# Performance work log

Hardware: AMD Instinct MI355X
Metric: run time of the kernel (lower is better)

## Reference

```python
import jax, jax.numpy as jnp
import numpy as np

N_HEADS = 8

def setup_inputs() -> dict:
    key = jax.random.key(0)
    qkv = jax.random.normal(key, (4, 1, 3 * N_HEADS * 64, 2048), dtype=jnp.float32)
    return {"qkv": qkv}

def reference(qkv):
    # qkv: [N, G, 3*H*C, T]
    bs, groups, width, length = qkv.shape
    ch = width // (3 * N_HEADS)
    q, k, v = jnp.split(qkv, 3, axis=2)
    scale = 1.0 / np.sqrt(ch)  # applied to BOTH q and k (as in original)
    qr = (q * scale).reshape(bs, groups, N_HEADS, ch, length)
    kr = (k * scale).reshape(bs, groups, N_HEADS, ch, length)
    vr = v.reshape(bs, groups, N_HEADS, ch, length)
    weight = jnp.einsum('bghct,bghcs->bghts', qr, kr)  # [N,G,H,T,T]
    weight = jax.nn.softmax(weight.astype(jnp.float32), axis=-1).astype(qkv.dtype)
    a = jnp.einsum('bghts,bghcs->bghct', weight, vr)  # [N,G,H,C,T]
    return a.reshape(bs, -1, length)  # [N, G*H*C, T]
```

## Files before the change

kernel.cpp:

```cpp
#include <hip/hip_runtime.h>
#include <hip/hip_bf16.h>

typedef __attribute__((ext_vector_type(4))) float f32x4;
typedef __attribute__((ext_vector_type(16))) float f32x16;
typedef __attribute__((ext_vector_type(4))) float f4;
typedef __attribute__((ext_vector_type(8))) short bf16x8;
typedef __attribute__((ext_vector_type(4))) short s16x4;
typedef __attribute__((ext_vector_type(4))) unsigned u32x4;

#define T_LEN 2048
#define SPAD 72
#define QSCALE 0.022542110013890054f

#define SWZ(r) (((r) ^ ((r) >> 3)) & 7)

__device__ inline short f2bf(float f) {
  unsigned u = __builtin_bit_cast(unsigned, f);
  return (short)((u + 0x7fffu + ((u >> 16) & 1u)) >> 16);
}

__global__ __launch_bounds__(256) void prep_t(const float* __restrict__ qkv,
                                              short* __restrict__ qt,
                                              short* __restrict__ kt) {
  __shared__ float tile[64][65];
  const int bid = blockIdx.x;
  const int tch = bid & 31;
  const int head = (bid >> 5) & 31;
  const int sel = bid >> 10;
  const int b = head >> 3, h = head & 7;
  const float* src = qkv + ((size_t)b * 1536 + sel * 512 + h * 64) * T_LEN + tch * 64;
  short* dst = (sel ? kt : qt) + (size_t)head * T_LEN * 64 + (size_t)tch * 64 * 64;
  const int tid = threadIdx.x;
  const float sc = sel ? 1.0f : QSCALE;

  for (int e = tid; e < 4096; e += 256) {
    int c = e >> 6, t = e & 63;
    tile[c][t] = src[(size_t)c * T_LEN + t];
  }
  __syncthreads();
  for (int e = tid; e < 2048; e += 256) {
    int t = e >> 5, c2 = (e & 31) * 2;
    unsigned lo = (unsigned short)f2bf(tile[c2][t] * sc);
    unsigned hi = (unsigned short)f2bf(tile[c2 + 1][t] * sc);
    int cdst = sel ? (c2 ^ (SWZ(t) << 3)) : c2;
    *(unsigned*)&dst[t * 64 + cdst] = lo | (hi << 16);
  }
}

__global__ __launch_bounds__(256) void prep_v(const float* __restrict__ qkv,
                                              short* __restrict__ v_out) {
  int id = blockIdx.x * 256 + threadIdx.x;
  int s4 = id & 15;
  int c = (id >> 4) & 63;
  int stile = (id >> 10) & 31;
  int head = id >> 15;
  int b = head >> 3, h = head & 7;
  const float* src =
      qkv + ((size_t)b * 1536 + 1024 + h * 64 + c) * T_LEN + stile * 64 + s4 * 4;
  f4 s = *(const f4*)src;
  s16x4 o;
#pragma unroll
  for (int j = 0; j < 4; ++j) o[j] = f2bf(s[j]);
  size_t dsts = (((size_t)head * 32 + stile) * 64 + c) * 64 + ((s4 * 4) ^ (SWZ(c) << 3));
  *(s16x4*)&v_out[dsts] = o;
}

__global__ __launch_bounds__(256, 2) void attn10(const short* __restrict__ Qt,
                                                 const short* __restrict__ Kt,
                                                 const short* __restrict__ Vb,
                                                 float* __restrict__ out) {
  __shared__ short KV[2][2][4096];

  const int bid = blockIdx.x;
  const int head = bid & 31;
  const int qblk = bid >> 5;

  const int tid = threadIdx.x;
  const int wave = tid >> 6;
  const int lane = tid & 63;
  const int l31 = lane & 31;
  const int hi = lane >> 5;

  const int t0 = qblk * 128 + wave * 32;

  const short* Qh = Qt + (size_t)head * 131072;
  const short* Kh = Kt + (size_t)head * 131072;
  const short* Vh = Vb + (size_t)head * 131072;
  float* O = out + (size_t)head * 131072;

  const int sw0 = SWZ(l31) << 3;
  const int sw1 = SWZ(l31 + 32) << 3;

  auto stage = [&](int buf, int it) {
#pragma unroll
    for (int j = 0; j < 4; ++j) {
      const int chunk = wave * 4 + j;
      const short* g = (chunk < 8 ? Kh : Vh) + it * 4096 + (chunk & 7) * 512 + lane * 8;
      short* l = &KV[buf][chunk >> 3][(chunk & 7) * 512];
      __builtin_amdgcn_global_load_lds((const __attribute__((address_space(1))) void*)g,
                                       (__attribute__((address_space(3))) void*)l,
                                       16, 0, 0);
    }
  };

  bf16x8 aq[4];
#pragma unroll
  for (int ck = 0; ck < 4; ++ck)
    aq[ck] = *(const bf16x8*)&Qh[(size_t)(t0 + l31) * 64 + ck * 16 + hi * 8];

  float l_lane = 0.f;
  f32x16 o_acc[2];
#pragma unroll
  for (int j = 0; j < 16; ++j) { o_acc[0][j] = 0.f; o_acc[1][j] = 0.f; }

  auto tile_body = [&](int buf) {
    f32x16 s0, s1;
#pragma unroll
    for (int j = 0; j < 16; ++j) { s0[j] = 0.f; s1[j] = 0.f; }
    __builtin_amdgcn_s_setprio(1);
#pragma unroll
    for (int ck = 0; ck < 4; ++ck) {
      const bf16x8 k0 = *(const bf16x8*)&KV[buf][0][l31 * 64 + ((ck * 16 + hi * 8) ^ sw0)];
      s0 = __builtin_amdgcn_mfma_f32_32x32x16_bf16(k0, aq[ck], s0, 0, 0, 0);
      const bf16x8 k1 = *(const bf16x8*)&KV[buf][0][(32 + l31) * 64 + ((ck * 16 + hi * 8) ^ sw1)];
      s1 = __builtin_amdgcn_mfma_f32_32x32x16_bf16(k1, aq[ck], s1, 0, 0, 0);
    }
    __builtin_amdgcn_s_setprio(0);

    float ps0 = 0.f, ps1 = 0.f, ps2 = 0.f, ps3 = 0.f;
    bf16x8 pf[4];
    const f32x16* sv[2] = {&s0, &s1};
#pragma unroll
    for (int sbk = 0; sbk < 2; ++sbk) {
      float p[16];
#pragma unroll
      for (int j = 0; j < 16; ++j) p[j] = __builtin_amdgcn_exp2f((*sv[sbk])[j]);
      ps0 += p[0] + p[4] + p[8] + p[12];
      ps1 += p[1] + p[5] + p[9] + p[13];
      ps2 += p[2] + p[6] + p[10] + p[14];
      ps3 += p[3] + p[7] + p[11] + p[15];
      unsigned w0, w1, w2, w3, w4, w5, w6, w7;
      asm("v_cvt_pk_bf16_f32 %0, %1, %2" : "=v"(w0) : "v"(p[0]), "v"(p[1]));
      asm("v_cvt_pk_bf16_f32 %0, %1, %2" : "=v"(w1) : "v"(p[2]), "v"(p[3]));
      asm("v_cvt_pk_bf16_f32 %0, %1, %2" : "=v"(w2) : "v"(p[4]), "v"(p[5]));
      asm("v_cvt_pk_bf16_f32 %0, %1, %2" : "=v"(w3) : "v"(p[6]), "v"(p[7]));
      asm("v_cvt_pk_bf16_f32 %0, %1, %2" : "=v"(w4) : "v"(p[8]), "v"(p[9]));
      asm("v_cvt_pk_bf16_f32 %0, %1, %2" : "=v"(w5) : "v"(p[10]), "v"(p[11]));
      asm("v_cvt_pk_bf16_f32 %0, %1, %2" : "=v"(w6) : "v"(p[12]), "v"(p[13]));
      asm("v_cvt_pk_bf16_f32 %0, %1, %2" : "=v"(w7) : "v"(p[14]), "v"(p[15]));
      asm("v_permlane32_swap_b32 %0, %1" : "+v"(w0), "+v"(w2));
      asm("v_permlane32_swap_b32 %0, %1" : "+v"(w1), "+v"(w3));
      asm("v_permlane32_swap_b32 %0, %1" : "+v"(w4), "+v"(w6));
      asm("v_permlane32_swap_b32 %0, %1" : "+v"(w5), "+v"(w7));
      u32x4 fe = {w0, w1, w2, w3};
      u32x4 fo = {w4, w5, w6, w7};
      pf[sbk * 2] = __builtin_bit_cast(bf16x8, fe);
      pf[sbk * 2 + 1] = __builtin_bit_cast(bf16x8, fo);
    }
    l_lane += (ps0 + ps1) + (ps2 + ps3);

    __builtin_amdgcn_s_setprio(1);
#pragma unroll
    for (int sc = 0; sc < 4; ++sc) {
      const bf16x8 v0 = *(const bf16x8*)&KV[buf][1][l31 * 64 + ((sc * 16 + hi * 8) ^ sw0)];
      o_acc[0] = __builtin_amdgcn_mfma_f32_32x32x16_bf16(v0, pf[sc], o_acc[0], 0, 0, 0);
      const bf16x8 v1 = *(const bf16x8*)&KV[buf][1][(32 + l31) * 64 + ((sc * 16 + hi * 8) ^ sw1)];
      o_acc[1] = __builtin_amdgcn_mfma_f32_32x32x16_bf16(v1, pf[sc], o_acc[1], 0, 0, 0);
    }
    __builtin_amdgcn_s_setprio(0);
  };

  stage(0, 0);
  __syncthreads();

  for (int itp = 0; itp < 16; ++itp) {
    const int it = itp * 2;
    stage(1, it + 1);
    tile_body(0);
    __syncthreads();
    if (it + 2 < 32) stage(0, it + 2);
    tile_body(1);
    __syncthreads();
  }

  const float l = l_lane + __shfl_xor(l_lane, 32, 64);
  const float rl = 1.0f / l;
#pragma unroll
  for (int ct = 0; ct < 2; ++ct)
#pragma unroll
    for (int j = 0; j < 16; ++j) {
      const int c = ct * 32 + (j & 3) + 8 * (j >> 2) + 4 * hi;
      O[(size_t)c * T_LEN + t0 + l31] = o_acc[ct][j] * rl;
    }
}

__global__ __launch_bounds__(256) void attn_fwd(const float* __restrict__ qkv,
                                                float* __restrict__ out) {
  __shared__ short KtS[64][SPAD];
  __shared__ short VtS[64][SPAD];
  __shared__ short PbS[4][16][SPAD];

  const int bid = blockIdx.x;
  const int qt = bid & 31;
  const int head = bid >> 5;
  const int b = head >> 3, h = head & 7;

  const size_t base = ((size_t)b * 1536 + h * 64) * T_LEN;
  const float* Q = qkv + base;
  const float* K = qkv + base + (size_t)512 * T_LEN;
  const float* V = qkv + base + (size_t)1024 * T_LEN;
  float* O = out + ((size_t)b * 512 + h * 64) * T_LEN;

  const int tid = threadIdx.x;
  const int wave = tid >> 6;
  const int lane = tid & 63;
  const int l15 = lane & 15;
  const int l4 = lane >> 4;
  const int t0 = qt * 64 + wave * 16;

  bf16x8 aq[2];
#pragma unroll
  for (int kk = 0; kk < 2; ++kk)
#pragma unroll
    for (int j = 0; j < 8; ++j) {
      int c = kk * 32 + l4 * 8 + j;
      aq[kk][j] = f2bf(Q[(size_t)c * T_LEN + t0 + l15]);
    }

  float m_run[4], l_run[4];
  f32x4 o_acc[4];
#pragma unroll
  for (int r = 0; r < 4; ++r) { m_run[r] = -1e30f; l_run[r] = 0.f; }
#pragma unroll
  for (int n = 0; n < 4; ++n) o_acc[n] = (f32x4){0.f, 0.f, 0.f, 0.f};

  const float inv64 = 0.015625f;

  for (int s0 = 0; s0 < T_LEN; s0 += 64) {
    __syncthreads();
    for (int e = tid; e < 4096; e += 256) {
      int c = e >> 6, s = e & 63;
      KtS[s][c] = f2bf(K[(size_t)c * T_LEN + s0 + s]);
      VtS[c][s] = f2bf(V[(size_t)c * T_LEN + s0 + s]);
    }
    __syncthreads();

    f32x4 sacc[4];
#pragma unroll
    for (int n = 0; n < 4; ++n) {
      const bf16x8 bk0 = *(const bf16x8*)&KtS[16 * n + l15][l4 * 8];
      const bf16x8 bk1 = *(const bf16x8*)&KtS[16 * n + l15][32 + l4 * 8];
      f32x4 z = (f32x4){0.f, 0.f, 0.f, 0.f};
      z = __builtin_amdgcn_mfma_f32_16x16x32_bf16(aq[0], bk0, z, 0, 0, 0);
      z = __builtin_amdgcn_mfma_f32_16x16x32_bf16(aq[1], bk1, z, 0, 0, 0);
      sacc[n] = z;
    }

#pragma unroll
    for (int r = 0; r < 4; ++r) {
      float mx = fmaxf(fmaxf(sacc[0][r], sacc[1][r]),
                       fmaxf(sacc[2][r], sacc[3][r])) * inv64;
#pragma unroll
      for (int off = 8; off >= 1; off >>= 1)
        mx = fmaxf(mx, __shfl_xor(mx, off, 64));
      const float m_new = fmaxf(m_run[r], mx);
      const float alpha = __expf(m_run[r] - m_new);
      float psum = 0.f;
#pragma unroll
      for (int n = 0; n < 4; ++n) {
        float p = __expf(sacc[n][r] * inv64 - m_new);
        psum += p;
        PbS[wave][l4 * 4 + r][16 * n + l15] = f2bf(p);
      }
#pragma unroll
      for (int off = 8; off >= 1; off >>= 1)
        psum += __shfl_xor(psum, off, 64);
      l_run[r] = l_run[r] * alpha + psum;
      m_run[r] = m_new;
#pragma unroll
      for (int n = 0; n < 4; ++n) o_acc[n][r] *= alpha;
    }

    const bf16x8 ap0 = *(const bf16x8*)&PbS[wave][l15][l4 * 8];
    const bf16x8 ap1 = *(const bf16x8*)&PbS[wave][l15][32 + l4 * 8];
#pragma unroll
    for (int n = 0; n < 4; ++n) {
      const bf16x8 bv0 = *(const bf16x8*)&VtS[16 * n + l15][l4 * 8];
      const bf16x8 bv1 = *(const bf16x8*)&VtS[16 * n + l15][32 + l4 * 8];
      o_acc[n] = __builtin_amdgcn_mfma_f32_16x16x32_bf16(ap0, bv0, o_acc[n], 0, 0, 0);
      o_acc[n] = __builtin_amdgcn_mfma_f32_16x16x32_bf16(ap1, bv1, o_acc[n], 0, 0, 0);
    }
  }

#pragma unroll
  for (int n = 0; n < 4; ++n)
#pragma unroll
    for (int r = 0; r < 4; ++r) {
      const int c = 16 * n + l15;
      const int t = t0 + l4 * 4 + r;
      O[(size_t)c * T_LEN + t] = o_acc[n][r] / l_run[r];
    }
}

extern "C" void kernel_launch(void* const* d_in, const int* in_sizes, int n_in,
                              void* d_out, int out_size, void* d_ws, size_t ws_size,
                              hipStream_t stream) {
  const float* qkv = (const float*)d_in[0];
  float* out = (float*)d_out;
  const size_t per_buf = (size_t)32 * T_LEN * 64;
  const size_t need = per_buf * 3 * sizeof(short);
  if (ws_size >= need) {
    short* qt = (short*)d_ws;
    short* kt = qt + per_buf;
    short* vb = kt + per_buf;
    hipLaunchKernelGGL(prep_t, dim3(2048), dim3(256), 0, stream, qkv, qt, kt);
    hipLaunchKernelGGL(prep_v, dim3(4096), dim3(256), 0, stream, qkv, vb);
    hipLaunchKernelGGL(attn10, dim3(512), dim3(256), 0, stream, qt, kt, vb, out);
  } else {
    hipLaunchKernelGGL(attn_fwd, dim3(1024), dim3(256), 0, stream, qkv, out);
  }
}
```

Baseline: 59.94 us.

## Process two 32-row query tiles per wave to reuse K/V fragments

Each wave now computes 64 query rows (two 32-row MFMA tiles) against every staged K/V tile, sharing each LDS K and V fragment load across both. The grid halves to 256 blocks of 256 queries and launch bounds drop to one block per CU. This cuts LDS reads and K/V staging per query but doubles accumulator registers and lowers occupancy, which may expose latency.

```diff
diff --git a/kernel.cpp b/kernel.cpp
--- a/kernel.cpp
+++ b/kernel.cpp
@@ -65,7 +65,7 @@
   *(s16x4*)&v_out[dsts] = o;
 }
 
-__global__ __launch_bounds__(256, 2) void attn10(const short* __restrict__ Qt,
+__global__ __launch_bounds__(256, 1) void attn11(const short* __restrict__ Qt,
                                                  const short* __restrict__ Kt,
                                                  const short* __restrict__ Vb,
                                                  float* __restrict__ out) {
@@ -81,7 +81,7 @@
   const int l31 = lane & 31;
   const int hi = lane >> 5;
 
-  const int t0 = qblk * 128 + wave * 32;
+  const int t0 = qblk * 256 + wave * 64;
 
   const short* Qh = Qt + (size_t)head * 131072;
   const short* Kh = Kt + (size_t)head * 131072;
@@ -103,32 +103,20 @@
     }
   };
 
-  bf16x8 aq[4];
-#pragma unroll
-  for (int ck = 0; ck < 4; ++ck)
-    aq[ck] = *(const bf16x8*)&Qh[(size_t)(t0 + l31) * 64 + ck * 16 + hi * 8];
-
-  float l_lane = 0.f;
-  f32x16 o_acc[2];
-#pragma unroll
-  for (int j = 0; j < 16; ++j) { o_acc[0][j] = 0.f; o_acc[1][j] = 0.f; }
-
-  auto tile_body = [&](int buf) {
-    f32x16 s0, s1;
-#pragma unroll
-    for (int j = 0; j < 16; ++j) { s0[j] = 0.f; s1[j] = 0.f; }
-    __builtin_amdgcn_s_setprio(1);
-#pragma unroll
-    for (int ck = 0; ck < 4; ++ck) {
-      const bf16x8 k0 = *(const bf16x8*)&KV[buf][0][l31 * 64 + ((ck * 16 + hi * 8) ^ sw0)];
-      s0 = __builtin_amdgcn_mfma_f32_32x32x16_bf16(k0, aq[ck], s0, 0, 0, 0);
-      const bf16x8 k1 = *(const bf16x8*)&KV[buf][0][(32 + l31) * 64 + ((ck * 16 + hi * 8) ^ sw1)];
-      s1 = __builtin_amdgcn_mfma_f32_32x32x16_bf16(k1, aq[ck], s1, 0, 0, 0);
-    }
-    __builtin_amdgcn_s_setprio(0);
-
+  bf16x8 aqA[4], aqB[4];
+#pragma unroll
+  for (int ck = 0; ck < 4; ++ck) {
+    aqA[ck] = *(const bf16x8*)&Qh[(size_t)(t0 + l31) * 64 + ck * 16 + hi * 8];
+    aqB[ck] = *(const bf16x8*)&Qh[(size_t)(t0 + 32 + l31) * 64 + ck * 16 + hi * 8];
+  }
+
+  float lA = 0.f, lB = 0.f;
+  f32x16 oA0, oA1, oB0, oB1;
+#pragma unroll
+  for (int j = 0; j < 16; ++j) { oA0[j] = 0.f; oA1[j] = 0.f; oB0[j] = 0.f; oB1[j] = 0.f; }
+
+  auto pack = [&](const f32x16& s0, const f32x16& s1, bf16x8(&pf)[4], float& l_acc) {
     float ps0 = 0.f, ps1 = 0.f, ps2 = 0.f, ps3 = 0.f;
-    bf16x8 pf[4];
     const f32x16* sv[2] = {&s0, &s1};
 #pragma unroll
     for (int sbk = 0; sbk < 2; ++sbk) {
@@ -157,15 +145,38 @@
       pf[sbk * 2] = __builtin_bit_cast(bf16x8, fe);
       pf[sbk * 2 + 1] = __builtin_bit_cast(bf16x8, fo);
     }
-    l_lane += (ps0 + ps1) + (ps2 + ps3);
+    l_acc += (ps0 + ps1) + (ps2 + ps3);
+  };
+
+  auto tile_body = [&](int buf) {
+    f32x16 sA0, sA1, sB0, sB1;
+#pragma unroll
+    for (int j = 0; j < 16; ++j) { sA0[j] = 0.f; sA1[j] = 0.f; sB0[j] = 0.f; sB1[j] = 0.f; }
+    __builtin_amdgcn_s_setprio(1);
+#pragma unroll
+    for (int ck = 0; ck < 4; ++ck) {
+      const bf16x8 k0 = *(const bf16x8*)&KV[buf][0][l31 * 64 + ((ck * 16 + hi * 8) ^ sw0)];
+      const bf16x8 k1 = *(const bf16x8*)&KV[buf][0][(32 + l31) * 64 + ((ck * 16 + hi * 8) ^ sw1)];
+      sA0 = __builtin_amdgcn_mfma_f32_32x32x16_bf16(k0, aqA[ck], sA0, 0, 0, 0);
+      sA1 = __builtin_amdgcn_mfma_f32_32x32x16_bf16(k1, aqA[ck], sA1, 0, 0, 0);
+      sB0 = __builtin_amdgcn_mfma_f32_32x32x16_bf16(k0, aqB[ck], sB0, 0, 0, 0);
+      sB1 = __builtin_amdgcn_mfma_f32_32x32x16_bf16(k1, aqB[ck], sB1, 0, 0, 0);
+    }
+    __builtin_amdgcn_s_setprio(0);
+
+    bf16x8 pfA[4], pfB[4];
+    pack(sA0, sA1, pfA, lA);
+    pack(sB0, sB1, pfB, lB);
 
     __builtin_amdgcn_s_setprio(1);
 #pragma unroll
     for (int sc = 0; sc < 4; ++sc) {
       const bf16x8 v0 = *(const bf16x8*)&KV[buf][1][l31 * 64 + ((sc * 16 + hi * 8) ^ sw0)];
-      o_acc[0] = __builtin_amdgcn_mfma_f32_32x32x16_bf16(v0, pf[sc], o_acc[0], 0, 0, 0);
       const bf16x8 v1 = *(const bf16x8*)&KV[buf][1][(32 + l31) * 64 + ((sc * 16 + hi * 8) ^ sw1)];
-      o_acc[1] = __builtin_amdgcn_mfma_f32_32x32x16_bf16(v1, pf[sc], o_acc[1], 0, 0, 0);
+      oA0 = __builtin_amdgcn_mfma_f32_32x32x16_bf16(v0, pfA[sc], oA0, 0, 0, 0);
+      oA1 = __builtin_amdgcn_mfma_f32_32x32x16_bf16(v1, pfA[sc], oA1, 0, 0, 0);
+      oB0 = __builtin_amdgcn_mfma_f32_32x32x16_bf16(v0, pfB[sc], oB0, 0, 0, 0);
+      oB1 = __builtin_amdgcn_mfma_f32_32x32x16_bf16(v1, pfB[sc], oB1, 0, 0, 0);
     }
     __builtin_amdgcn_s_setprio(0);
   };
@@ -183,15 +194,18 @@
     __syncthreads();
   }
 
-  const float l = l_lane + __shfl_xor(l_lane, 32, 64);
-  const float rl = 1.0f / l;
-#pragma unroll
-  for (int ct = 0; ct < 2; ++ct)
-#pragma unroll
-    for (int j = 0; j < 16; ++j) {
-      const int c = ct * 32 + (j & 3) + 8 * (j >> 2) + 4 * hi;
-      O[(size_t)c * T_LEN + t0 + l31] = o_acc[ct][j] * rl;
-    }
+  const float lAt = lA + __shfl_xor(lA, 32, 64);
+  const float lBt = lB + __shfl_xor(lB, 32, 64);
+  const float rlA = 1.0f / lAt;
+  const float rlB = 1.0f / lBt;
+#pragma unroll
+  for (int j = 0; j < 16; ++j) {
+    const int c0 = (j & 3) + 8 * (j >> 2) + 4 * hi;
+    O[(size_t)c0 * T_LEN + t0 + l31] = oA0[j] * rlA;
+    O[(size_t)(32 + c0) * T_LEN + t0 + l31] = oA1[j] * rlA;
+    O[(size_t)c0 * T_LEN + t0 + 32 + l31] = oB0[j] * rlB;
+    O[(size_t)(32 + c0) * T_LEN + t0 + 32 + l31] = oB1[j] * rlB;
+  }
 }
 
 __global__ __launch_bounds__(256) void attn_fwd(const float* __restrict__ qkv,
@@ -315,7 +329,7 @@
     short* vb = kt + per_buf;
     hipLaunchKernelGGL(prep_t, dim3(2048), dim3(256), 0, stream, qkv, qt, kt);
     hipLaunchKernelGGL(prep_v, dim3(4096), dim3(256), 0, stream, qkv, vb);
-    hipLaunchKernelGGL(attn10, dim3(512), dim3(256), 0, stream, qt, kt, vb, out);
+    hipLaunchKernelGGL(attn11, dim3(256), dim3(256), 0, stream, qt, kt, vb, out);
   } else {
     hipLaunchKernelGGL(attn_fwd, dim3(1024), dim3(256), 0, stream, qkv, out);
   }
```

Result: slower. 69.08 us (+15.3%).

## Split key sequence across two wave groups per block with LDS reduction

Applied to the files above, without the earlier changes.

The attention kernel now uses 512-thread blocks. Two groups of four waves each process half of the key/value tiles for the same 128 queries, and each group keeps its own double-buffered LDS staging. At the end, group 1 writes its partial output accumulators and row sums to LDS, and group 0 combines them and normalizes. The aim is to double the number of waves per CU for better latency hiding and MFMA utilization. The cost is twice the LDS footprint, possible register pressure under launch_bounds(512,4), and an extra reduction step through shared memory.

```diff
diff --git a/kernel.cpp b/kernel.cpp
--- a/kernel.cpp
+++ b/kernel.cpp
@@ -65,11 +65,11 @@
   *(s16x4*)&v_out[dsts] = o;
 }
 
-__global__ __launch_bounds__(256, 2) void attn10(const short* __restrict__ Qt,
+__global__ __launch_bounds__(512, 4) void attn13(const short* __restrict__ Qt,
                                                  const short* __restrict__ Kt,
                                                  const short* __restrict__ Vb,
                                                  float* __restrict__ out) {
-  __shared__ short KV[2][2][4096];
+  __shared__ short KV[2][2][2][4096];
 
   const int bid = blockIdx.x;
   const int head = bid & 31;
@@ -77,11 +77,14 @@
 
   const int tid = threadIdx.x;
   const int wave = tid >> 6;
+  const int grp = wave >> 2;
+  const int wv = wave & 3;
   const int lane = tid & 63;
   const int l31 = lane & 31;
   const int hi = lane >> 5;
 
-  const int t0 = qblk * 128 + wave * 32;
+  const int t0 = qblk * 128 + wv * 32;
+  const int sbase = grp * 16;
 
   const short* Qh = Qt + (size_t)head * 131072;
   const short* Kh = Kt + (size_t)head * 131072;
@@ -94,9 +97,10 @@
   auto stage = [&](int buf, int it) {
 #pragma unroll
     for (int j = 0; j < 4; ++j) {
-      const int chunk = wave * 4 + j;
-      const short* g = (chunk < 8 ? Kh : Vh) + it * 4096 + (chunk & 7) * 512 + lane * 8;
-      short* l = &KV[buf][chunk >> 3][(chunk & 7) * 512];
+      const int chunk = wv * 4 + j;
+      const short* g =
+          (chunk < 8 ? Kh : Vh) + (sbase + it) * 4096 + (chunk & 7) * 512 + lane * 8;
+      short* l = &KV[grp][buf][chunk >> 3][(chunk & 7) * 512];
       __builtin_amdgcn_global_load_lds((const __attribute__((address_space(1))) void*)g,
                                        (__attribute__((address_space(3))) void*)l,
                                        16, 0, 0);
@@ -120,9 +124,9 @@
     __builtin_amdgcn_s_setprio(1);
 #pragma unroll
     for (int ck = 0; ck < 4; ++ck) {
-      const bf16x8 k0 = *(const bf16x8*)&KV[buf][0][l31 * 64 + ((ck * 16 + hi * 8) ^ sw0)];
+      const bf16x8 k0 = *(const bf16x8*)&KV[grp][buf][0][l31 * 64 + ((ck * 16 + hi * 8) ^ sw0)];
       s0 = __builtin_amdgcn_mfma_f32_32x32x16_bf16(k0, aq[ck], s0, 0, 0, 0);
-      const bf16x8 k1 = *(const bf16x8*)&KV[buf][0][(32 + l31) * 64 + ((ck * 16 + hi * 8) ^ sw1)];
+      const bf16x8 k1 = *(const bf16x8*)&KV[grp][buf][0][(32 + l31) * 64 + ((ck * 16 + hi * 8) ^ sw1)];
       s1 = __builtin_amdgcn_mfma_f32_32x32x16_bf16(k1, aq[ck], s1, 0, 0, 0);
     }
     __builtin_amdgcn_s_setprio(0);
@@ -162,9 +166,9 @@
     __builtin_amdgcn_s_setprio(1);
 #pragma unroll
     for (int sc = 0; sc < 4; ++sc) {
-      const bf16x8 v0 = *(const bf16x8*)&KV[buf][1][l31 * 64 + ((sc * 16 + hi * 8) ^ sw0)];
+      const bf16x8 v0 = *(const bf16x8*)&KV[grp][buf][1][l31 * 64 + ((sc * 16 + hi * 8) ^ sw0)];
       o_acc[0] = __builtin_amdgcn_mfma_f32_32x32x16_bf16(v0, pf[sc], o_acc[0], 0, 0, 0);
-      const bf16x8 v1 = *(const bf16x8*)&KV[buf][1][(32 + l31) * 64 + ((sc * 16 + hi * 8) ^ sw1)];
+      const bf16x8 v1 = *(const bf16x8*)&KV[grp][buf][1][(32 + l31) * 64 + ((sc * 16 + hi * 8) ^ sw1)];
       o_acc[1] = __builtin_amdgcn_mfma_f32_32x32x16_bf16(v1, pf[sc], o_acc[1], 0, 0, 0);
     }
     __builtin_amdgcn_s_setprio(0);
@@ -173,25 +177,35 @@
   stage(0, 0);
   __syncthreads();
 
-  for (int itp = 0; itp < 16; ++itp) {
+  for (int itp = 0; itp < 8; ++itp) {
     const int it = itp * 2;
     stage(1, it + 1);
     tile_body(0);
     __syncthreads();
-    if (it + 2 < 32) stage(0, it + 2);
+    if (itp < 7) stage(0, it + 2);
     tile_body(1);
     __syncthreads();
   }
 
-  const float l = l_lane + __shfl_xor(l_lane, 32, 64);
-  const float rl = 1.0f / l;
-#pragma unroll
-  for (int ct = 0; ct < 2; ++ct)
+  const float lg = l_lane + __shfl_xor(l_lane, 32, 64);
+  float* xb = (float*)&KV[0][0][0][0];
+  if (grp == 1) {
+    float* dst = xb + (wv * 64 + lane) * 33;
+#pragma unroll
+    for (int j = 0; j < 16; ++j) { dst[j] = o_acc[0][j]; dst[16 + j] = o_acc[1][j]; }
+    dst[32] = lg;
+  }
+  __syncthreads();
+  if (grp == 0) {
+    const float* src = xb + (wv * 64 + lane) * 33;
+    const float rl = 1.0f / (lg + src[32]);
 #pragma unroll
     for (int j = 0; j < 16; ++j) {
-      const int c = ct * 32 + (j & 3) + 8 * (j >> 2) + 4 * hi;
-      O[(size_t)c * T_LEN + t0 + l31] = o_acc[ct][j] * rl;
-    }
+      const int c0 = (j & 3) + 8 * (j >> 2) + 4 * hi;
+      O[(size_t)c0 * T_LEN + t0 + l31] = (o_acc[0][j] + src[j]) * rl;
+      O[(size_t)(32 + c0) * T_LEN + t0 + l31] = (o_acc[1][j] + src[16 + j]) * rl;
+    }
+  }
 }
 
 __global__ __launch_bounds__(256) void attn_fwd(const float* __restrict__ qkv,
@@ -315,7 +329,7 @@
     short* vb = kt + per_buf;
     hipLaunchKernelGGL(prep_t, dim3(2048), dim3(256), 0, stream, qkv, qt, kt);
     hipLaunchKernelGGL(prep_v, dim3(4096), dim3(256), 0, stream, qkv, vb);
-    hipLaunchKernelGGL(attn10, dim3(512), dim3(256), 0, stream, qt, kt, vb, out);
+    hipLaunchKernelGGL(attn13, dim3(512), dim3(512), 0, stream, qt, kt, vb, out);
   } else {
     hipLaunchKernelGGL(attn_fwd, dim3(1024), dim3(256), 0, stream, qkv, out);
   }
```

Result: faster. 58.40 us (-2.6%).
